# Kernel tuning notes

Hardware: AMD Instinct MI355X
Metric: run time of the kernel (lower is better)

Reference implementation:

```python
import jax, jax.numpy as jnp
import numpy as np
from jax import lax

NUM_GROUP = 512
GROUP_SIZE = 32
ENC_CH = 384
BN_EPS = 1e-5


def setup_inputs() -> dict:
    key = jax.random.key(0)
    ks = jax.random.split(key, 8)
    B, N = 16, 8192
    def w(k, o, i):
        return jax.random.normal(k, (o, i), jnp.float32) * (1.0 / np.sqrt(i))
    return {
        "xyz": jax.random.normal(ks[0], (B, N, 3), jnp.float32),
        # first_conv: Conv1d(3,128,1)+BN+ReLU, Conv1d(128,256,1)
        "w1": w(ks[1], 128, 3), "b1": jnp.zeros((128,), jnp.float32),
        "g1": jnp.ones((128,), jnp.float32), "bt1": jnp.zeros((128,), jnp.float32),
        "w2": w(ks[2], 256, 128), "b2": jnp.zeros((256,), jnp.float32),
        # second_conv: Conv1d(512,512,1)+BN+ReLU, Conv1d(512,encoder_channel,1)
        "w3": w(ks[3], 512, 512), "b3": jnp.zeros((512,), jnp.float32),
        "g3": jnp.ones((512,), jnp.float32), "bt3": jnp.zeros((512,), jnp.float32),
        "w4": w(ks[4], ENC_CH, 512), "b4": jnp.zeros((ENC_CH,), jnp.float32),
    }


def fps(xyz, npoint):
    """Farthest point sampling. xyz: [B,N,3] -> indices [B,npoint]."""
    B, N, _ = xyz.shape
    def step(carry, _):
        dist, farthest = carry                       # [B,N], [B]
        centroid = jnp.take_along_axis(xyz, farthest[:, None, None], axis=1)  # [B,1,3]
        d = jnp.sum((xyz - centroid) ** 2, axis=-1)  # [B,N]
        dist = jnp.minimum(dist, d)
        nxt = jnp.argmax(dist, axis=-1)
        return (dist, nxt), farthest
    init = (jnp.full((B, N), 1e10, xyz.dtype), jnp.zeros((B,), jnp.int32))
    _, idxs = lax.scan(step, init, None, length=npoint)
    return idxs.T  # [B,npoint]


def knn_point(nsample, xyz, new_xyz):
    """new_xyz [B,S,3], xyz [B,N,3] -> [B,S,nsample] indices of nearest pts."""
    d = (-2.0 * jnp.einsum('bsc,bnc->bsn', new_xyz, xyz)
         + jnp.sum(new_xyz ** 2, -1)[:, :, None]
         + jnp.sum(xyz ** 2, -1)[:, None, :])
    _, idx = lax.top_k(-d, nsample)
    return idx


def batch_norm(x, gamma, beta):
    # x: [M, L, C]; training-mode BN over (M, L) per channel
    mean = jnp.mean(x, axis=(0, 1), keepdims=True)
    var = jnp.var(x, axis=(0, 1), keepdims=True)
    return (x - mean) * lax.rsqrt(var + BN_EPS) * gamma + beta


def reference(xyz, w1, b1, g1, bt1, w2, b2, w3, b3, g3, bt3, w4, b4):
    B, N, _ = xyz.shape
    G, K = NUM_GROUP, GROUP_SIZE
    # ---- Group: FPS centers + kNN neighborhoods, centered ----
    cidx = fps(xyz, G)                                          # [B,G]
    center = jnp.take_along_axis(xyz, cidx[:, :, None], axis=1) # [B,G,3]
    idx = knn_point(K, xyz, center)                             # [B,G,K]
    nb = jnp.take_along_axis(xyz, idx.reshape(B, G * K, 1), axis=1)
    nb = nb.reshape(B, G, K, 3) - center[:, :, None, :]         # [B,G,K,3]
    # ---- Encoder (PointNet stem), 1x1 conv == channel matmul ----
    pg = nb.reshape(B * G, K, 3)                                # [BG,K,3]
    f = jnp.einsum('mkc,oc->mko', pg, w1) + b1                  # [BG,K,128]
    f = jax.nn.relu(batch_norm(f, g1, bt1))
    f = jnp.einsum('mkc,oc->mko', f, w2) + b2                   # [BG,K,256]
    fg = jnp.max(f, axis=1, keepdims=True)                      # [BG,1,256]
    f = jnp.concatenate([jnp.broadcast_to(fg, f.shape), f], axis=-1)  # [BG,K,512]
    f = jnp.einsum('mkc,oc->mko', f, w3) + b3
    f = jax.nn.relu(batch_norm(f, g3, bt3))
    f = jnp.einsum('mkc,oc->mko', f, w4) + b4                   # [BG,K,C]
    feat = jnp.max(f, axis=1)                                   # [BG,C]
    return feat.reshape(B, G, ENC_CH)
```

## Files before the change

### kernel.cpp

```cpp
#include <hip/hip_runtime.h>
#include <cstddef>

#define B_   16
#define N_   8192
#define G_   512
#define K_   32
#define GT   8192
#define NROW 262144
#define EPS  1e-5f

typedef unsigned short ushort_t;
typedef short bf16x8 __attribute__((ext_vector_type(8)));
typedef float f32x4  __attribute__((ext_vector_type(4)));

constexpr size_t OFF_CENTERS = 0;
constexpr size_t OFF_NB      = OFF_CENTERS + 24576;
constexpr size_t OFF_FG      = OFF_NB      + 786432;
constexpr size_t OFF_C1      = OFF_FG      + 2097152;
constexpr size_t OFF_MOM     = OFF_C1      + 1048576;
constexpr size_t OFF_A       = OFF_MOM     + 16;
constexpr size_t OFF_S1      = OFF_A       + 16384;
constexpr size_t OFF_SF      = OFF_S1      + 128;
constexpr size_t OFF_MU      = OFF_SF      + 256;
constexpr size_t OFF_W2S1    = OFF_MU      + 512;
constexpr size_t OFF_BN1A    = OFF_W2S1    + 256;
constexpr size_t OFF_BN1D    = OFF_BN1A    + 128;
constexpr size_t OFF_BN3A    = OFF_BN1D    + 128;
constexpr size_t OFF_BN3D    = OFF_BN3A    + 512;
constexpr size_t OFF_SFF     = OFF_BN3D    + 512;
constexpr size_t OFF_PFCT    = OFF_SFF     + 65536;
constexpr size_t OFF_T1      = OFF_PFCT    + 32768;
constexpr size_t OFF_SCCW    = OFF_T1      + 32768;
constexpr size_t OFF_SFC     = OFF_SCCW    + 65536;
constexpr size_t OFF_W2T     = OFF_SFC     + 65536;
constexpr size_t OFF_W3T     = OFF_W2T     + 32768;
constexpr size_t OFF_W4H     = OFF_W3T     + 262144;
constexpr size_t OFF_W4L     = OFF_W4H     + 98304;
constexpr size_t OFF_APART   = OFF_W4L     + 98304;
constexpr size_t OFF_W23     = OFF_APART   + 8388608;
constexpr size_t OFF_W23H    = OFF_W23     + 65536;
constexpr size_t OFF_W23L    = OFF_W23H    + 32768;
constexpr size_t OFF_W2H     = OFF_W23L    + 32768;
constexpr size_t OFF_W2L     = OFF_W2H     + 16384;
constexpr size_t WS_FLOATS   = OFF_W2L     + 16384;
constexpr size_t OFF_BASE3   = OFF_APART;

__device__ __forceinline__ unsigned bf16_rne(float v) {
    unsigned u = __float_as_uint(v);
    return (u + 0x7fffu + ((u >> 16) & 1u)) >> 16;
}

__global__ __launch_bounds__(1024) void fps_kernel(const float* __restrict__ xyz,
                                                   float* __restrict__ centers) {
    int b = blockIdx.x, t = threadIdx.x;
    const float* xb = xyz + (size_t)b * N_ * 3;
    float px[8], py[8], pz[8], dist[8];
#pragma unroll
    for (int i = 0; i < 8; ++i) {
        int p = t + (i << 10);
        px[i] = xb[p*3]; py[i] = xb[p*3+1]; pz[i] = xb[p*3+2];
        dist[i] = 1e10f;
    }
    __shared__ float redV[2][16];
    __shared__ int   redI[2][16];
    __shared__ float cxyz[2][3];
    if (t == 0) { cxyz[0][0] = px[0]; cxyz[0][1] = py[0]; cxyz[0][2] = pz[0]; }
    __syncthreads();
    for (int it = 0; it < G_; ++it) {
        int cur = it & 1;
        float lcx = cxyz[cur][0], lcy = cxyz[cur][1], lcz = cxyz[cur][2];
        if (t == 0) {
            float* cd = centers + ((size_t)b * G_ + it) * 3;
            cd[0] = lcx; cd[1] = lcy; cd[2] = lcz;
        }
        float bv = -1.0f; int bp = 0;
#pragma unroll
        for (int i = 0; i < 8; ++i) {
            float dx = __fsub_rn(px[i], lcx);
            float dy = __fsub_rn(py[i], lcy);
            float dz = __fsub_rn(pz[i], lcz);
            float d  = __fadd_rn(__fadd_rn(__fmul_rn(dx,dx), __fmul_rn(dy,dy)), __fmul_rn(dz,dz));
            float nd = fminf(dist[i], d);
            dist[i] = nd;
            if (nd > bv) { bv = nd; bp = t + (i << 10); }
        }
#pragma unroll
        for (int off = 1; off < 64; off <<= 1) {
            float ov = __shfl_xor(bv, off);
            int   op = __shfl_xor(bp, off);
            if (ov > bv || (ov == bv && op < bp)) { bv = ov; bp = op; }
        }
        if ((t & 63) == 0) { redV[cur][t >> 6] = bv; redI[cur][t >> 6] = bp; }
        __syncthreads();
        float v = redV[cur][t & 15]; int p = redI[cur][t & 15];
#pragma unroll
        for (int off = 1; off < 16; off <<= 1) {
            float ov = __shfl_xor(v, off);
            int   op = __shfl_xor(p, off);
            if (ov > v || (ov == v && op < p)) { v = ov; p = op; }
        }
        if ((p & 1023) == t) {
            int i = p >> 10;
            cxyz[cur ^ 1][0] = px[i]; cxyz[cur ^ 1][1] = py[i]; cxyz[cur ^ 1][2] = pz[i];
        }
        __syncthreads();
    }
}

__global__ __launch_bounds__(256) void knn_kernel(const float* __restrict__ xyz,
                                                  const float* __restrict__ centers,
                                                  float* __restrict__ nb) {
    int g = blockIdx.x, t = threadIdx.x;
    int b = g >> 9;
    const float* xb = xyz + (size_t)b * N_ * 3;
    const float* c  = centers + (size_t)g * 3;
    float lcx = c[0], lcy = c[1], lcz = c[2];
    float cn2 = __fadd_rn(__fadd_rn(__fmul_rn(lcx,lcx), __fmul_rn(lcy,lcy)), __fmul_rn(lcz,lcz));
    float dreg[32];
#pragma unroll 8
    for (int i = 0; i < 32; ++i) {
        int p = t + (i << 8);
        float x = xb[p*3], y = xb[p*3+1], z = xb[p*3+2];
        float pn2 = __fadd_rn(__fadd_rn(__fmul_rn(x,x), __fmul_rn(y,y)), __fmul_rn(z,z));
        float dot = __fadd_rn(__fadd_rn(__fmul_rn(lcx,x), __fmul_rn(lcy,y)), __fmul_rn(lcz,z));
        dreg[i]   = __fadd_rn(__fadd_rn(__fmul_rn(-2.0f,dot), cn2), pn2);
    }
    __shared__ float redV[2][4];
    __shared__ int   redI[2][4];
    int myp = 0;
    for (int s = 0; s < K_; ++s) {
        float bv = 1e30f; int bp = 0;
#pragma unroll
        for (int i = 0; i < 32; ++i) {
            float v = dreg[i];
            if (v < bv) { bv = v; bp = t + (i << 8); }
        }
#pragma unroll
        for (int off = 1; off < 64; off <<= 1) {
            float ov = __shfl_xor(bv, off);
            int   op = __shfl_xor(bp, off);
            if (ov < bv || (ov == bv && op < bp)) { bv = ov; bp = op; }
        }
        int buf = s & 1;
        if ((t & 63) == 0) { redV[buf][t >> 6] = bv; redI[buf][t >> 6] = bp; }
        __syncthreads();
        float v = redV[buf][0]; int p = redI[buf][0];
#pragma unroll
        for (int w = 1; w < 4; ++w) {
            float ov = redV[buf][w]; int op = redI[buf][w];
            if (ov < v || (ov == v && op < p)) { v = ov; p = op; }
        }
        if (s == t) myp = p;
#pragma unroll
        for (int i = 0; i < 32; ++i)
            if (p == t + (i << 8)) dreg[i] = 1e30f;
    }
    if (t < K_) {
        int p = myp;
        float* dst = nb + ((size_t)g * K_ + t) * 3;
        dst[0] = xb[p*3]   - lcx;
        dst[1] = xb[p*3+1] - lcy;
        dst[2] = xb[p*3+2] - lcz;
    }
}

__global__ void zero_mom_kernel(float* __restrict__ mom) {
    if (threadIdx.x < 16) mom[threadIdx.x] = 0.0f;
}

__global__ void moments_kernel(const float* __restrict__ nb, float* __restrict__ mom) {
    int idx = blockIdx.x * 256 + threadIdx.x;
    float x = nb[idx*3], y = nb[idx*3+1], z = nb[idx*3+2];
    float v[9] = {x, y, z, x*x, y*y, z*z, x*y, x*z, y*z};
    __shared__ float red[4][9];
    int t = threadIdx.x;
#pragma unroll
    for (int q = 0; q < 9; ++q) {
        float s = v[q];
#pragma unroll
        for (int off = 32; off; off >>= 1) s += __shfl_xor(s, off);
        if ((t & 63) == 0) red[t >> 6][q] = s;
    }
    __syncthreads();
    if (t < 9) atomicAdd(&mom[t], red[0][t] + red[1][t] + red[2][t] + red[3][t]);
}

__global__ void bn1_params_kernel(const float* __restrict__ mom,
                                  const float* __restrict__ w1, const float* __restrict__ b1,
                                  const float* __restrict__ g1, const float* __restrict__ bt1,
                                  float* __restrict__ bn1a, float* __restrict__ bn1d) {
    int c = threadIdx.x;
    const float inv_n = 1.0f / (float)NROW;
    float mx = mom[0]*inv_n, my = mom[1]*inv_n, mz = mom[2]*inv_n;
    float cxx = mom[3]*inv_n - mx*mx, cyy = mom[4]*inv_n - my*my, czz = mom[5]*inv_n - mz*mz;
    float cxy = mom[6]*inv_n - mx*my, cxz = mom[7]*inv_n - mx*mz, cyz = mom[8]*inv_n - my*mz;
    float wx = w1[c*3], wy = w1[c*3+1], wz = w1[c*3+2];
    float mean = wx*mx + wy*my + wz*mz + b1[c];
    float var  = wx*wx*cxx + wy*wy*cyy + wz*wz*czz
               + 2.0f*(wx*wy*cxy + wx*wz*cxz + wy*wz*cyz);
    float a = rsqrtf(var + EPS) * g1[c];
    bn1a[c] = a;
    bn1d[c] = (b1[c] - mean) * a + bt1[c];
}

__global__ void transpose_kernel(float* __restrict__ out, const float* __restrict__ in, int R, int C) {
    int t = blockIdx.x * blockDim.x + threadIdx.x;
    if (t < R * C) {
        int i = t / C, j = t % C;
        out[(size_t)j * R + i] = in[t];
    }
}

__global__ void split_kernel(const float* __restrict__ src, ushort_t* __restrict__ hi,
                             ushort_t* __restrict__ lo, int n) {
    int i = blockIdx.x * 256 + threadIdx.x;
    if (i < n) {
        float v = src[i];
        unsigned h = bf16_rne(v);
        hi[i] = (ushort_t)h;
        float r = v - __uint_as_float(h << 16);
        lo[i] = (ushort_t)bf16_rne(r);
    }
}

__global__ __launch_bounds__(256) void p1_mfma_kernel(
        const float* __restrict__ nbg, const float* __restrict__ w1,
        const float* __restrict__ bn1a, const float* __restrict__ bn1d,
        const ushort_t* __restrict__ w2h, const ushort_t* __restrict__ w2l,
        const float* __restrict__ b2,
        float* __restrict__ fg, float* __restrict__ c1,
        float* __restrict__ apart) {
    __shared__ short f1h[32*128], f1l[32*128];
    __shared__ short f1Th[128*40], f1Tl[128*40];
    __shared__ float c1part[2][128];
    __shared__ float nbs[96];
    int t = threadIdx.x;
    int lane = t & 63, w = t >> 6;
    int l15 = lane & 15, lh = lane >> 4;

    f32x4 accA[2][8];
#pragma unroll
    for (int i2 = 0; i2 < 2; ++i2)
#pragma unroll
        for (int j = 0; j < 8; ++j) accA[i2][j] = (f32x4){0.f, 0.f, 0.f, 0.f};

    for (int gi = 0; gi < 16; ++gi) {
        int g = blockIdx.x * 16 + gi;
        if (gi == 0 && t < 96) nbs[t] = nbg[(size_t)g * 96 + t];
        __syncthreads();
        {
            int ch = t & 127, rh = t >> 7;
            float a = bn1a[ch], d = bn1d[ch];
            float w0 = w1[ch*3], wa = w1[ch*3+1], wb = w1[ch*3+2];
            float csum = 0.f;
#pragma unroll
            for (int rr = 0; rr < 16; rr += 2) {
                int r0 = rh*16 + rr;
                unsigned hp[2], lp[2];
#pragma unroll
                for (int u = 0; u < 2; ++u) {
                    int r = r0 + u;
                    float x = nbs[r*3], y = nbs[r*3+1], z = nbs[r*3+2];
                    float m = __fmul_rn(x, w0);
                    m = __fmaf_rn(y, wa, m);
                    m = __fmaf_rn(z, wb, m);
                    m = __fmaf_rn(m, a, d);
                    m = fmaxf(m, 0.f);
                    csum = __fadd_rn(csum, m);
                    unsigned h = bf16_rne(m);
                    unsigned l = bf16_rne(m - __uint_as_float(h << 16));
                    hp[u] = h; lp[u] = l;
                    int off = r*256 + ((ch*2) ^ ((r&7)<<4));
                    *(short*)((char*)f1h + off) = (short)h;
                    *(short*)((char*)f1l + off) = (short)l;
                }
                int offT = ch*80 + r0*2;
                *(unsigned*)((char*)f1Th + offT) = hp[0] | (hp[1] << 16);
                *(unsigned*)((char*)f1Tl + offT) = lp[0] | (lp[1] << 16);
            }
            c1part[rh][ch] = csum;
        }
        __syncthreads();
        if (t < 128) c1[(size_t)g*128 + t] = __fadd_rn(c1part[0][t], c1part[1][t]);
        if (gi < 15 && t < 96) nbs[t] = nbg[(size_t)(g+1) * 96 + t];

#pragma unroll
        for (int ci = 0; ci < 4; ++ci) {
            int ct = w*4 + ci;
            f32x4 acc2[2];
            acc2[0] = (f32x4){0.f,0.f,0.f,0.f};
            acc2[1] = (f32x4){0.f,0.f,0.f,0.f};
#pragma unroll
            for (int kq = 0; kq < 4; ++kq) {
                size_t wo = (size_t)(ct*16 + l15)*128 + kq*32 + lh*8;
                bf16x8 wah = *(const bf16x8*)(w2h + wo);
                bf16x8 wal = *(const bf16x8*)(w2l + wo);
#pragma unroll
                for (int pt = 0; pt < 2; ++pt) {
                    int row = pt*16 + l15;
                    int off = row*256 + ((kq*64 + lh*16) ^ ((row&7)<<4));
                    bf16x8 fbh = *(bf16x8*)((char*)f1h + off);
                    bf16x8 fbl = *(bf16x8*)((char*)f1l + off);
                    acc2[pt] = __builtin_amdgcn_mfma_f32_16x16x32_bf16(wah, fbh, acc2[pt], 0, 0, 0);
                    acc2[pt] = __builtin_amdgcn_mfma_f32_16x16x32_bf16(wah, fbl, acc2[pt], 0, 0, 0);
                    acc2[pt] = __builtin_amdgcn_mfma_f32_16x16x32_bf16(wal, fbh, acc2[pt], 0, 0, 0);
                }
            }
            f32x4 mx;
#pragma unroll
            for (int q = 0; q < 4; ++q) mx[q] = fmaxf(acc2[0][q], acc2[1][q]);
#pragma unroll
            for (int off = 1; off < 16; off <<= 1) {
#pragma unroll
                for (int q = 0; q < 4; ++q) mx[q] = fmaxf(mx[q], __shfl_xor(mx[q], off));
            }
            if (l15 == 0) {
                int cb = ct*16 + lh*4;
#pragma unroll
                for (int q = 0; q < 4; ++q)
                    fg[(size_t)g*256 + cb + q] = mx[q] + b2[cb + q];
            }
        }

        {
            bf16x8 ahA[2], alA[2];
#pragma unroll
            for (int i2 = 0; i2 < 2; ++i2) {
                int chi = (2*w + i2)*16 + l15;
                int offA = chi*80 + lh*16;
                ahA[i2] = *(bf16x8*)((char*)f1Th + offA);
                alA[i2] = *(bf16x8*)((char*)f1Tl + offA);
            }
#pragma unroll
            for (int j = 0; j < 8; ++j) {
                int chj = j*16 + l15;
                int offB = chj*80 + lh*16;
                bf16x8 bh = *(bf16x8*)((char*)f1Th + offB);
                bf16x8 bl = *(bf16x8*)((char*)f1Tl + offB);
#pragma unroll
                for (int i2 = 0; i2 < 2; ++i2) {
                    accA[i2][j] = __builtin_amdgcn_mfma_f32_16x16x32_bf16(ahA[i2], bh, accA[i2][j], 0, 0, 0);
                    accA[i2][j] = __builtin_amdgcn_mfma_f32_16x16x32_bf16(ahA[i2], bl, accA[i2][j], 0, 0, 0);
                    accA[i2][j] = __builtin_amdgcn_mfma_f32_16x16x32_bf16(alA[i2], bh, accA[i2][j], 0, 0, 0);
                }
            }
        }
    }
    float* ap = apart + (size_t)blockIdx.x * 16384;
#pragma unroll
    for (int i2 = 0; i2 < 2; ++i2)
#pragma unroll
        for (int j = 0; j < 8; ++j)
#pragma unroll
            for (int q = 0; q < 4; ++q)
                ap[((2*w + i2)*16 + lh*4 + q)*128 + j*16 + l15] = accA[i2][j][q];
}

__global__ void reduce_a_kernel(const float* __restrict__ apart, float* __restrict__ A) {
    int e = blockIdx.x * 256 + threadIdx.x;
    float s = 0.f;
    for (int b = 0; b < 512; ++b) s = __fadd_rn(s, apart[(size_t)b * 16384 + e]);
    A[e] = s;
}

__global__ void reduce_cf_kernel(const float* __restrict__ c1, const float* __restrict__ fgb,
                                 float* __restrict__ s1, float* __restrict__ sf) {
    int c = blockIdx.x, t = threadIdx.x;
    __shared__ float red[256];
    float s = 0.f;
    if (c < 128) { for (int g = t; g < GT; g += 256) s += c1[(size_t)g*128 + c]; }
    else { int cc = c - 128; for (int g = t; g < GT; g += 256) s += fgb[(size_t)g*256 + cc]; }
    red[t] = s; __syncthreads();
    for (int w = 128; w; w >>= 1) { if (t < w) red[t] += red[t + w]; __syncthreads(); }
    if (t == 0) { if (c < 128) s1[c] = red[0]; else sf[c - 128] = red[0]; }
}

__global__ void assemble_mu_kernel(const float* __restrict__ s1, const float* __restrict__ sf,
                                   const float* __restrict__ w2t, const float* __restrict__ b2,
                                   float* __restrict__ mu, float* __restrict__ w2s1) {
    int t = blockIdx.x * 256 + threadIdx.x;
    const float inv_n = 1.0f / (float)NROW;
    if (t < 256) {
        mu[t] = sf[t] * (1.0f / (float)GT);
    } else {
        int c = t - 256;
        float s = 0.f;
        for (int k = 0; k < 128; ++k) s = __fmaf_rn(w2t[k*256 + c], s1[k], s);
        w2s1[c] = s;
        mu[t] = (s + (float)NROW * b2[c]) * inv_n;
    }
}

__global__ __launch_bounds__(256) void gemm_tn_kernel(float* __restrict__ Cm,
                                                      const float* __restrict__ Am, const float* __restrict__ Bm,
                                                      int M, int N, int Kd, int lda, int ldb) {
    __shared__ float As[16][17], Bs[16][17];
    int tx = threadIdx.x & 15, ty = threadIdx.x >> 4;
    int j = blockIdx.x * 16 + tx;
    int i = blockIdx.y * 16 + ty;
    float acc = 0.f;
    for (int k0 = 0; k0 < Kd; k0 += 16) {
        As[ty][tx] = Am[(size_t)(k0 + ty) * lda + blockIdx.y*16 + tx];
        Bs[ty][tx] = Bm[(size_t)(k0 + ty) * ldb + blockIdx.x*16 + tx];
        __syncthreads();
#pragma unroll
        for (int kk = 0; kk < 16; ++kk) acc = __fmaf_rn(As[kk][ty], Bs[kk][tx], acc);
        __syncthreads();
    }
    Cm[(size_t)i * N + j] = acc;
}

__global__ __launch_bounds__(256) void gemm_nn_kernel(float* __restrict__ Cm,
                                                      const float* __restrict__ Am, const float* __restrict__ Bm,
                                                      int M, int N, int Kd, int lda, int ldb) {
    __shared__ float As[16][65], Bs[16][65];
    int t = threadIdx.x;
    int i0 = blockIdx.y * 64, j0 = blockIdx.x * 64;
    int tx = t & 15, ty = t >> 4;
    int lr = t & 63, lk = t >> 6;
    float acc[4][4];
#pragma unroll
    for (int a = 0; a < 4; ++a)
#pragma unroll
        for (int b = 0; b < 4; ++b) acc[a][b] = 0.f;
    for (int k0 = 0; k0 < Kd; k0 += 16) {
#pragma unroll
        for (int u = 0; u < 4; ++u) {
            int k = lk*4 + u;
            As[k][lr] = Am[(size_t)(i0 + lr) * lda + k0 + k];
            Bs[k][lr] = Bm[(size_t)(k0 + k) * ldb + j0 + lr];
        }
        __syncthreads();
#pragma unroll
        for (int kk = 0; kk < 16; ++kk) {
            float av[4], bv[4];
#pragma unroll
            for (int u = 0; u < 4; ++u) av[u] = As[kk][ty*4+u];
#pragma unroll
            for (int u = 0; u < 4; ++u) bv[u] = Bs[kk][tx*4+u];
#pragma unroll
            for (int a = 0; a < 4; ++a)
#pragma unroll
                for (int b = 0; b < 4; ++b) acc[a][b] = __fmaf_rn(av[a], bv[b], acc[a][b]);
        }
        __syncthreads();
    }
#pragma unroll
    for (int a = 0; a < 4; ++a)
#pragma unroll
        for (int b = 0; b < 4; ++b)
            Cm[(size_t)(i0 + ty*4 + a) * N + j0 + tx*4 + b] = acc[a][b];
}

__global__ __launch_bounds__(256) void bn3_params_kernel(const float* __restrict__ w3, const float* __restrict__ b3,
        const float* __restrict__ g3, const float* __restrict__ bt3,
        const float* __restrict__ sff, const float* __restrict__ sfc, const float* __restrict__ sccw,
        const float* __restrict__ sf, const float* __restrict__ w2s1, const float* __restrict__ b2,
        const float* __restrict__ mu, float* __restrict__ bn3a, float* __restrict__ bn3d) {
    int c = blockIdx.x, t = threadIdx.x;
    __shared__ float wL[512];
    __shared__ float red[256];
    wL[t]       = w3[(size_t)c*512 + t];
    wL[256 + t] = w3[(size_t)c*512 + 256 + t];
    __syncthreads();
    float v1 = 0.f, v2 = 0.f, v3 = 0.f;
    for (int i = 0; i < 256; ++i) {
        float wfi = wL[i], wci = wL[256 + i];
        v1 = __fmaf_rn(wfi, sff[(size_t)i*256 + t], v1);
        v2 = __fmaf_rn(wfi, sfc[(size_t)i*256 + t], v2);
        v3 = __fmaf_rn(wci, sccw[(size_t)i*256 + t], v3);
    }
    float wf_t = wL[t], wc_t = wL[256 + t];
    float vals[7];
    vals[0] = v1 * wf_t;
    vals[1] = v2 * wc_t;
    vals[2] = v3 * wc_t;
    vals[3] = wf_t * sf[t];
    vals[4] = wc_t * b2[t];
    vals[5] = wc_t * w2s1[t];
    vals[6] = wf_t * mu[t] + wc_t * mu[256 + t];
    float sums[7];
    for (int q = 0; q < 7; ++q) {
        red[t] = vals[q]; __syncthreads();
        for (int w = 128; w; w >>= 1) { if (t < w) red[t] += red[t + w]; __syncthreads(); }
        sums[q] = red[0]; __syncthreads();
    }
    if (t == 0) {
        float n = (float)NROW;
        float Q = 32.f*sums[0] + 2.f*(sums[1] + 32.f*sums[3]*sums[4])
                + sums[2] + 2.f*sums[5]*sums[4] + n*sums[4]*sums[4];
        float m3 = sums[6] + b3[c];
        float E2 = Q / n + 2.f*b3[c]*sums[6] + b3[c]*b3[c];
        float var = E2 - m3*m3;
        float a = rsqrtf(var + EPS) * g3[c];
        bn3a[c] = a;
        bn3d[c] = (b3[c] + sums[4] - m3) * a + bt3[c];
    }
}

__global__ __launch_bounds__(512) void p3_mfma_kernel(
        const float* __restrict__ nbg, const float* __restrict__ w1,
        const float* __restrict__ bn1a, const float* __restrict__ bn1d,
        const ushort_t* __restrict__ w23h, const ushort_t* __restrict__ w23l,
        const ushort_t* __restrict__ w4h, const ushort_t* __restrict__ w4l,
        const float* __restrict__ base3, const float* __restrict__ bn3a, const float* __restrict__ bn3d,
        const float* __restrict__ b4, float* __restrict__ out) {
    __shared__ short f1h[64*128], f1l[64*128];
    __shared__ short f3h[64*64],  f3l[64*64];
    __shared__ float nbs[192];
    int t = threadIdx.x;
    int g0 = blockIdx.x * 2;
    if (t < 192) nbs[t] = nbg[(size_t)g0 * 96 + t];
    __syncthreads();
    {
        int cp = t & 63;
        int r0 = (t >> 6) * 8;
        int c0 = cp * 2;
        float w00=w1[c0*3+0], w01=w1[c0*3+1], w02=w1[c0*3+2];
        float w10=w1[c0*3+3], w11=w1[c0*3+4], w12=w1[c0*3+5];
        float aA=bn1a[c0], dA=bn1d[c0], aB=bn1a[c0+1], dB=bn1d[c0+1];
#pragma unroll
        for (int rr = 0; rr < 8; ++rr) {
            int r = r0 + rr;
            float x = nbs[r*3], y = nbs[r*3+1], z = nbs[r*3+2];
            float mA = __fmul_rn(x, w00); mA = __fmaf_rn(y, w01, mA); mA = __fmaf_rn(z, w02, mA);
            mA = __fmaf_rn(mA, aA, dA); mA = fmaxf(mA, 0.f);
            float mB = __fmul_rn(x, w10); mB = __fmaf_rn(y, w11, mB); mB = __fmaf_rn(z, w12, mB);
            mB = __fmaf_rn(mB, aB, dB); mB = fmaxf(mB, 0.f);
            unsigned hA = bf16_rne(mA), hB = bf16_rne(mB);
            unsigned lA = bf16_rne(mA - __uint_as_float(hA << 16));
            unsigned lB = bf16_rne(mB - __uint_as_float(hB << 16));
            int off = r*256 + ((cp*4) ^ ((r&7)<<4));
            *(unsigned*)((char*)f1h + off) = hA | (hB << 16);
            *(unsigned*)((char*)f1l + off) = lA | (lB << 16);
        }
    }
    int lane = t & 63, w = t >> 6;
    int l15 = lane & 15, lh = lane >> 4;
    int m3c  = (w & 3) * 16;
    int m3rg = w >> 2;
    int m4g = w >> 2, m4n = (w & 3) * 96;

    f32x4 acc4[2][6];
#pragma unroll
    for (int mt = 0; mt < 2; ++mt)
#pragma unroll
        for (int nt = 0; nt < 6; ++nt) acc4[mt][nt] = (f32x4){0.f, 0.f, 0.f, 0.f};

    const float* b3p = base3 + (size_t)(g0 + m3rg) * 512 + m3c + lh * 4;
    f32x4 b3cur = *(const f32x4*)b3p;
    __syncthreads();

    for (int chunk = 0; chunk < 8; ++chunk) {
        f32x4 b3nxt = b3cur;
        if (chunk < 7) b3nxt = *(const f32x4*)(b3p + (chunk + 1) * 64);
        f32x4 acc3[2];
        acc3[0] = b3cur; acc3[1] = b3cur;
#pragma unroll
        for (int ks = 0; ks < 4; ++ks) {
            size_t wo = (size_t)(chunk*64 + m3c + l15) * 128 + ks*32 + lh*8;
            bf16x8 wah = *(const bf16x8*)(w23h + wo);
            bf16x8 wal = *(const bf16x8*)(w23l + wo);
#pragma unroll
            for (int nt = 0; nt < 2; ++nt) {
                int row = m3rg*32 + nt*16 + l15;
                int off = row*256 + ((ks*64 + lh*16) ^ ((row&7)<<4));
                bf16x8 fbh = *(bf16x8*)((char*)f1h + off);
                bf16x8 fbl = *(bf16x8*)((char*)f1l + off);
                acc3[nt] = __builtin_amdgcn_mfma_f32_16x16x32_bf16(wah, fbh, acc3[nt], 0, 0, 0);
                acc3[nt] = __builtin_amdgcn_mfma_f32_16x16x32_bf16(wah, fbl, acc3[nt], 0, 0, 0);
                acc3[nt] = __builtin_amdgcn_mfma_f32_16x16x32_bf16(wal, fbh, acc3[nt], 0, 0, 0);
            }
        }
        __syncthreads();
        {
            int cb = chunk*64 + m3c + lh*4;
            f32x4 a4 = *(const f32x4*)(bn3a + cb);
            f32x4 d4 = *(const f32x4*)(bn3d + cb);
#pragma unroll
            for (int nt = 0; nt < 2; ++nt) {
                int row = m3rg*32 + nt*16 + l15;
                unsigned hw0, hw1, lw0, lw1;
                {
                    float v0 = fmaxf(__fmaf_rn(acc3[nt][0], a4[0], d4[0]), 0.f);
                    float v1 = fmaxf(__fmaf_rn(acc3[nt][1], a4[1], d4[1]), 0.f);
                    float v2 = fmaxf(__fmaf_rn(acc3[nt][2], a4[2], d4[2]), 0.f);
                    float v3 = fmaxf(__fmaf_rn(acc3[nt][3], a4[3], d4[3]), 0.f);
                    unsigned h0 = bf16_rne(v0), h1 = bf16_rne(v1), h2 = bf16_rne(v2), h3 = bf16_rne(v3);
                    unsigned l0 = bf16_rne(v0 - __uint_as_float(h0 << 16));
                    unsigned l1 = bf16_rne(v1 - __uint_as_float(h1 << 16));
                    unsigned l2 = bf16_rne(v2 - __uint_as_float(h2 << 16));
                    unsigned l3 = bf16_rne(v3 - __uint_as_float(h3 << 16));
                    hw0 = h0 | (h1 << 16); hw1 = h2 | (h3 << 16);
                    lw0 = l0 | (l1 << 16); lw1 = l2 | (l3 << 16);
                }
                int off = row*128 + (((m3c + lh*4) * 2) ^ ((row&7)<<4));
                *(unsigned long long*)((char*)f3h + off) = (unsigned long long)hw0 | ((unsigned long long)hw1 << 32);
                *(unsigned long long*)((char*)f3l + off) = (unsigned long long)lw0 | ((unsigned long long)lw1 << 32);
            }
        }
        __syncthreads();
#pragma unroll
        for (int ks = 0; ks < 2; ++ks) {
            bf16x8 fah[2], fal[2];
#pragma unroll
            for (int mt = 0; mt < 2; ++mt) {
                int row = m4g*32 + mt*16 + l15;
                int off = row*128 + ((ks*64 + lh*16) ^ ((row&7)<<4));
                fah[mt] = *(bf16x8*)((char*)f3h + off);
                fal[mt] = *(bf16x8*)((char*)f3l + off);
            }
#pragma unroll
            for (int nt = 0; nt < 6; ++nt) {
                int n = m4n + nt*16 + l15;
                size_t wo = (size_t)n*512 + chunk*64 + ks*32 + lh*8;
                bf16x8 wbh = *(const bf16x8*)(w4h + wo);
                bf16x8 wbl = *(const bf16x8*)(w4l + wo);
#pragma unroll
                for (int mt = 0; mt < 2; ++mt) {
                    acc4[mt][nt] = __builtin_amdgcn_mfma_f32_16x16x32_bf16(fah[mt], wbh, acc4[mt][nt], 0, 0, 0);
                    acc4[mt][nt] = __builtin_amdgcn_mfma_f32_16x16x32_bf16(fah[mt], wbl, acc4[mt][nt], 0, 0, 0);
                    acc4[mt][nt] = __builtin_amdgcn_mfma_f32_16x16x32_bf16(fal[mt], wbh, acc4[mt][nt], 0, 0, 0);
                }
            }
        }
        b3cur = b3nxt;
    }
    int gg = g0 + m4g;
#pragma unroll
    for (int nt = 0; nt < 6; ++nt) {
        int n = m4n + nt*16 + l15;
        float m = acc4[0][nt][0];
#pragma unroll
        for (int q = 1; q < 4; ++q) m = fmaxf(m, acc4[0][nt][q]);
#pragma unroll
        for (int q = 0; q < 4; ++q) m = fmaxf(m, acc4[1][nt][q]);
        m = fmaxf(m, __shfl_xor(m, 16));
        m = fmaxf(m, __shfl_xor(m, 32));
        if (lh == 0) out[(size_t)gg * 384 + n] = m + b4[n];
    }
}

extern "C" void kernel_launch(void* const* d_in, const int* in_sizes, int n_in,
                              void* d_out, int out_size, void* d_ws, size_t ws_size,
                              hipStream_t stream) {
    const float* xyz = (const float*)d_in[0];
    const float* w1  = (const float*)d_in[1];
    const float* b1  = (const float*)d_in[2];
    const float* g1  = (const float*)d_in[3];
    const float* bt1 = (const float*)d_in[4];
    const float* w2  = (const float*)d_in[5];
    const float* b2  = (const float*)d_in[6];
    const float* w3  = (const float*)d_in[7];
    const float* b3  = (const float*)d_in[8];
    const float* g3  = (const float*)d_in[9];
    const float* bt3 = (const float*)d_in[10];
    const float* w4  = (const float*)d_in[11];
    const float* b4  = (const float*)d_in[12];
    float* out = (float*)d_out;
    float* ws  = (float*)d_ws;

    if (ws_size < WS_FLOATS * sizeof(float)) return;

    float* centers = ws + OFF_CENTERS;
    float* nb      = ws + OFF_NB;
    float* fgB     = ws + OFF_FG;
    float* c1B     = ws + OFF_C1;
    float* mom     = ws + OFF_MOM;
    float* A       = ws + OFF_A;
    float* s1      = ws + OFF_S1;
    float* sf      = ws + OFF_SF;
    float* mu      = ws + OFF_MU;
    float* w2s1    = ws + OFF_W2S1;
    float* bn1a    = ws + OFF_BN1A;
    float* bn1d    = ws + OFF_BN1D;
    float* bn3a    = ws + OFF_BN3A;
    float* bn3d    = ws + OFF_BN3D;
    float* sff     = ws + OFF_SFF;
    float* pfct    = ws + OFF_PFCT;
    float* t1m     = ws + OFF_T1;
    float* sccw    = ws + OFF_SCCW;
    float* sfcm    = ws + OFF_SFC;
    float* w2t     = ws + OFF_W2T;
    float* w3t     = ws + OFF_W3T;
    ushort_t* w4h  = (ushort_t*)(ws + OFF_W4H);
    ushort_t* w4l  = (ushort_t*)(ws + OFF_W4L);
    float* apart   = ws + OFF_APART;
    float* w23     = ws + OFF_W23;
    ushort_t* w23h = (ushort_t*)(ws + OFF_W23H);
    ushort_t* w23l = (ushort_t*)(ws + OFF_W23L);
    ushort_t* w2h  = (ushort_t*)(ws + OFF_W2H);
    ushort_t* w2l  = (ushort_t*)(ws + OFF_W2L);
    float* base3   = ws + OFF_BASE3;

    zero_mom_kernel<<<1, 64, 0, stream>>>(mom);
    fps_kernel<<<B_, 1024, 0, stream>>>(xyz, centers);
    knn_kernel<<<GT, 256, 0, stream>>>(xyz, centers, nb);
    moments_kernel<<<NROW/256, 256, 0, stream>>>(nb, mom);
    bn1_params_kernel<<<1, 128, 0, stream>>>(mom, w1, b1, g1, bt1, bn1a, bn1d);
    transpose_kernel<<<(256*128 + 255)/256, 256, 0, stream>>>(w2t, w2, 256, 128);
    transpose_kernel<<<(512*512 + 255)/256, 256, 0, stream>>>(w3t, w3, 512, 512);
    gemm_tn_kernel<<<dim3(8, 32), 256, 0, stream>>>(w23, w3t + 256*512, w2, 512, 128, 256, 512, 128);
    split_kernel<<<(65536 + 255)/256, 256, 0, stream>>>(w23, w23h, w23l, 65536);
    split_kernel<<<(196608 + 255)/256, 256, 0, stream>>>(w4, w4h, w4l, 196608);
    split_kernel<<<(32768 + 255)/256, 256, 0, stream>>>(w2, w2h, w2l, 32768);
    p1_mfma_kernel<<<512, 256, 0, stream>>>(nb, w1, bn1a, bn1d, w2h, w2l, b2, fgB, c1B, apart);
    reduce_a_kernel<<<64, 256, 0, stream>>>(apart, A);
    gemm_nn_kernel<<<dim3(8, 128), 256, 0, stream>>>(base3, fgB, w3t, GT, 512, 256, 256, 512);
    reduce_cf_kernel<<<384, 256, 0, stream>>>(c1B, fgB, s1, sf);
    assemble_mu_kernel<<<2, 256, 0, stream>>>(s1, sf, w2t, b2, mu, w2s1);
    gemm_tn_kernel<<<dim3(16,16), 256, 0, stream>>>(sff,  fgB,  fgB, 256, 256, GT,  256, 256);
    gemm_tn_kernel<<<dim3(16, 8), 256, 0, stream>>>(pfct, c1B,  fgB, 128, 256, GT,  128, 256);
    gemm_tn_kernel<<<dim3(16, 8), 256, 0, stream>>>(t1m,  A,    w2t, 128, 256, 128, 128, 256);
    gemm_tn_kernel<<<dim3(16,16), 256, 0, stream>>>(sccw, w2t,  t1m, 256, 256, 128, 256, 256);
    gemm_tn_kernel<<<dim3(16,16), 256, 0, stream>>>(sfcm, pfct, w2t, 256, 256, 128, 256, 256);
    bn3_params_kernel<<<512, 256, 0, stream>>>(w3, b3, g3, bt3, sff, sfcm, sccw, sf, w2s1, b2, mu, bn3a, bn3d);
    p3_mfma_kernel<<<GT/2, 512, 0, stream>>>(nb, w1, bn1a, bn1d, w23h, w23l, w4h, w4l,
                                             base3, bn3a, bn3d, b4, out);
}
```

Measured before the change: 3.195 ms.

## Cache per-thread KNN minima, double-buffer f3 tiles, add MFMA priority hints

In the KNN kernel each thread keeps its running minimum and rescans its 32 distances only when its own point was selected, instead of rescanning every round. The final MLP kernel double-buffers the f3 shared tiles, which removes one barrier per chunk, and reads neighbour coordinates straight from global memory instead of staging them in shared memory. s_setprio hints are placed around the MFMA loops in two kernels to favour matrix-issuing waves. Together these cut redundant VALU work and barrier stalls, at the cost of more shared memory per block, which may lower occupancy.

```diff
diff --git a/kernel.cpp b/kernel.cpp
--- a/kernel.cpp
+++ b/kernel.cpp
@@ -117,24 +117,22 @@
     float lcx = c[0], lcy = c[1], lcz = c[2];
     float cn2 = __fadd_rn(__fadd_rn(__fmul_rn(lcx,lcx), __fmul_rn(lcy,lcy)), __fmul_rn(lcz,lcz));
     float dreg[32];
+    float bvt = 1e30f; int bpt = 0;
 #pragma unroll 8
     for (int i = 0; i < 32; ++i) {
         int p = t + (i << 8);
         float x = xb[p*3], y = xb[p*3+1], z = xb[p*3+2];
         float pn2 = __fadd_rn(__fadd_rn(__fmul_rn(x,x), __fmul_rn(y,y)), __fmul_rn(z,z));
         float dot = __fadd_rn(__fadd_rn(__fmul_rn(lcx,x), __fmul_rn(lcy,y)), __fmul_rn(lcz,z));
-        dreg[i]   = __fadd_rn(__fadd_rn(__fmul_rn(-2.0f,dot), cn2), pn2);
+        float d   = __fadd_rn(__fadd_rn(__fmul_rn(-2.0f,dot), cn2), pn2);
+        dreg[i] = d;
+        if (d < bvt) { bvt = d; bpt = p; }
     }
     __shared__ float redV[2][4];
     __shared__ int   redI[2][4];
     int myp = 0;
     for (int s = 0; s < K_; ++s) {
-        float bv = 1e30f; int bp = 0;
-#pragma unroll
-        for (int i = 0; i < 32; ++i) {
-            float v = dreg[i];
-            if (v < bv) { bv = v; bp = t + (i << 8); }
-        }
+        float bv = bvt; int bp = bpt;
 #pragma unroll
         for (int off = 1; off < 64; off <<= 1) {
             float ov = __shfl_xor(bv, off);
@@ -151,9 +149,17 @@
             if (ov < v || (ov == v && op < p)) { v = ov; p = op; }
         }
         if (s == t) myp = p;
-#pragma unroll
-        for (int i = 0; i < 32; ++i)
-            if (p == t + (i << 8)) dreg[i] = 1e30f;
+        if ((p & 255) == t) {
+#pragma unroll
+            for (int i = 0; i < 32; ++i)
+                if (p == t + (i << 8)) dreg[i] = 1e30f;
+            bvt = 1e30f; bpt = t;
+#pragma unroll
+            for (int i = 0; i < 32; ++i) {
+                float vv = dreg[i];
+                if (vv < bvt) { bvt = vv; bpt = t + (i << 8); }
+            }
+        }
     }
     if (t < K_) {
         int p = myp;
@@ -290,6 +296,7 @@
             f32x4 acc2[2];
             acc2[0] = (f32x4){0.f,0.f,0.f,0.f};
             acc2[1] = (f32x4){0.f,0.f,0.f,0.f};
+            __builtin_amdgcn_s_setprio(1);
 #pragma unroll
             for (int kq = 0; kq < 4; ++kq) {
                 size_t wo = (size_t)(ct*16 + l15)*128 + kq*32 + lh*8;
@@ -306,6 +313,7 @@
                     acc2[pt] = __builtin_amdgcn_mfma_f32_16x16x32_bf16(wal, fbh, acc2[pt], 0, 0, 0);
                 }
             }
+            __builtin_amdgcn_s_setprio(0);
             f32x4 mx;
 #pragma unroll
             for (int q = 0; q < 4; ++q) mx[q] = fmaxf(acc2[0][q], acc2[1][q]);
@@ -331,6 +339,7 @@
                 ahA[i2] = *(bf16x8*)((char*)f1Th + offA);
                 alA[i2] = *(bf16x8*)((char*)f1Tl + offA);
             }
+            __builtin_amdgcn_s_setprio(1);
 #pragma unroll
             for (int j = 0; j < 8; ++j) {
                 int chj = j*16 + l15;
@@ -344,6 +353,7 @@
                     accA[i2][j] = __builtin_amdgcn_mfma_f32_16x16x32_bf16(alA[i2], bh, accA[i2][j], 0, 0, 0);
                 }
             }
+            __builtin_amdgcn_s_setprio(0);
         }
     }
     float* ap = apart + (size_t)blockIdx.x * 16384;
@@ -506,23 +516,21 @@
         const float* __restrict__ base3, const float* __restrict__ bn3a, const float* __restrict__ bn3d,
         const float* __restrict__ b4, float* __restrict__ out) {
     __shared__ short f1h[64*128], f1l[64*128];
-    __shared__ short f3h[64*64],  f3l[64*64];
-    __shared__ float nbs[192];
+    __shared__ short f3h[2][64*64], f3l[2][64*64];
     int t = threadIdx.x;
     int g0 = blockIdx.x * 2;
-    if (t < 192) nbs[t] = nbg[(size_t)g0 * 96 + t];
-    __syncthreads();
     {
         int cp = t & 63;
         int r0 = (t >> 6) * 8;
         int c0 = cp * 2;
+        const float* nbp = nbg + (size_t)g0 * 96;
         float w00=w1[c0*3+0], w01=w1[c0*3+1], w02=w1[c0*3+2];
         float w10=w1[c0*3+3], w11=w1[c0*3+4], w12=w1[c0*3+5];
         float aA=bn1a[c0], dA=bn1d[c0], aB=bn1a[c0+1], dB=bn1d[c0+1];
 #pragma unroll
         for (int rr = 0; rr < 8; ++rr) {
             int r = r0 + rr;
-            float x = nbs[r*3], y = nbs[r*3+1], z = nbs[r*3+2];
+            float x = nbp[r*3], y = nbp[r*3+1], z = nbp[r*3+2];
             float mA = __fmul_rn(x, w00); mA = __fmaf_rn(y, w01, mA); mA = __fmaf_rn(z, w02, mA);
             mA = __fmaf_rn(mA, aA, dA); mA = fmaxf(mA, 0.f);
             float mB = __fmul_rn(x, w10); mB = __fmaf_rn(y, w11, mB); mB = __fmaf_rn(z, w12, mB);
@@ -554,8 +562,11 @@
     for (int chunk = 0; chunk < 8; ++chunk) {
         f32x4 b3nxt = b3cur;
         if (chunk < 7) b3nxt = *(const f32x4*)(b3p + (chunk + 1) * 64);
+        short* f3hb = &f3h[chunk & 1][0];
+        short* f3lb = &f3l[chunk & 1][0];
         f32x4 acc3[2];
         acc3[0] = b3cur; acc3[1] = b3cur;
+        __builtin_amdgcn_s_setprio(1);
 #pragma unroll
         for (int ks = 0; ks < 4; ++ks) {
             size_t wo = (size_t)(chunk*64 + m3c + l15) * 128 + ks*32 + lh*8;
@@ -572,7 +583,7 @@
                 acc3[nt] = __builtin_amdgcn_mfma_f32_16x16x32_bf16(wal, fbh, acc3[nt], 0, 0, 0);
             }
         }
-        __syncthreads();
+        __builtin_amdgcn_s_setprio(0);
         {
             int cb = chunk*64 + m3c + lh*4;
             f32x4 a4 = *(const f32x4*)(bn3a + cb);
@@ -595,11 +606,12 @@
                     lw0 = l0 | (l1 << 16); lw1 = l2 | (l3 << 16);
                 }
                 int off = row*128 + (((m3c + lh*4) * 2) ^ ((row&7)<<4));
-                *(unsigned long long*)((char*)f3h + off) = (unsigned long long)hw0 | ((unsigned long long)hw1 << 32);
-                *(unsigned long long*)((char*)f3l + off) = (unsigned long long)lw0 | ((unsigned long long)lw1 << 32);
-            }
-        }
-        __syncthreads();
+                *(unsigned long long*)((char*)f3hb + off) = (unsigned long long)hw0 | ((unsigned long long)hw1 << 32);
+                *(unsigned long long*)((char*)f3lb + off) = (unsigned long long)lw0 | ((unsigned long long)lw1 << 32);
+            }
+        }
+        __syncthreads();
+        __builtin_amdgcn_s_setprio(1);
 #pragma unroll
         for (int ks = 0; ks < 2; ++ks) {
             bf16x8 fah[2], fal[2];
@@ -607,8 +619,8 @@
             for (int mt = 0; mt < 2; ++mt) {
                 int row = m4g*32 + mt*16 + l15;
                 int off = row*128 + ((ks*64 + lh*16) ^ ((row&7)<<4));
-                fah[mt] = *(bf16x8*)((char*)f3h + off);
-                fal[mt] = *(bf16x8*)((char*)f3l + off);
+                fah[mt] = *(bf16x8*)((char*)f3hb + off);
+                fal[mt] = *(bf16x8*)((char*)f3lb + off);
             }
 #pragma unroll
             for (int nt = 0; nt < 6; ++nt) {
@@ -624,6 +636,7 @@
                 }
             }
         }
+        __builtin_amdgcn_s_setprio(0);
         b3cur = b3nxt;
     }
     int gg = g0 + m4g;
```

Measured after the change: 3.140 ms. No clear change (-1.7%).
